# Kernel tuning notes

Hardware: AMD Instinct MI355X
Metric: run time of the kernel (lower is better)

Reference implementation:

```python
import jax, jax.numpy as jnp
import numpy as np

NUM_HEADS = 16
EPS = 1e-5


def _layernorm(x, gamma, beta):
    # LayerNorm over last dim (head_dim), biased variance as in torch
    mu = jnp.mean(x, axis=-1, keepdims=True)
    var = jnp.mean(jnp.square(x - mu), axis=-1, keepdims=True)
    return (x - mu) * jax.lax.rsqrt(var + EPS) * gamma + beta


def setup_inputs() -> dict:
    key = jax.random.key(0)
    ks = jax.random.split(key, 10)
    B, T, C = 16, 2048, 1024
    Bk = 4
    Dh = C // NUM_HEADS
    w = 0.02
    return {
        "q": jax.random.normal(ks[0], (B, T, C), jnp.float32),
        "k": jax.random.normal(ks[1], (Bk, T, C), jnp.float32),
        "v": jax.random.normal(ks[2], (Bk, T, C), jnp.float32),
        "Wq": jax.random.normal(ks[3], (C, C), jnp.float32) * w,
        "Wk": jax.random.normal(ks[4], (C, C), jnp.float32) * w,
        "Wv": jax.random.normal(ks[5], (C, C), jnp.float32) * w,
        "Wo": jax.random.normal(ks[6], (C, C), jnp.float32) * w,
        "bo": jnp.zeros((C,), jnp.float32),
        "gamma": jnp.ones((Dh,), jnp.float32),
        "beta": jnp.zeros((Dh,), jnp.float32),
    }


def reference(q, k, v, Wq, Wk, Wv, Wo, bo, gamma, beta):
    B, N, C = q.shape
    H = NUM_HEADS
    Dh = C // H
    scale = 8.0 / Dh  # use_mup=True

    reps = B // k.shape[0]
    k = jnp.tile(k, (reps, 1, 1))[:, :N]
    v = jnp.tile(v, (reps, 1, 1))[:, :N]

    # torch Linear: x @ W.T  (no qkv bias)
    qp = jnp.einsum("bnc,dc->bnd", q, Wq).reshape(B, N, H, Dh)
    kp = jnp.einsum("bnc,dc->bnd", k, Wk).reshape(B, N, H, Dh)
    vp = jnp.einsum("bnc,dc->bnd", v, Wv).reshape(B, N, H, Dh)

    qp = _layernorm(qp, gamma, beta) * scale
    kp = _layernorm(kp, gamma, beta)

    # Faithful to source: NO head permute before matmul -> per-token (H,H) attention
    attn = jnp.einsum("bnhd,bngd->bnhg", qp, kp)  # [B,N,H,H]
    attn = jax.nn.softmax(attn, axis=-1)
    x = jnp.einsum("bnhg,bngd->bnhd", attn, vp)  # [B,N,H,Dh]
    # torch: transpose(1,2).reshape(B,N,C)
    x = x.transpose(0, 2, 1, 3).reshape(B, N, C)
    return jnp.einsum("bnc,dc->bnd", x, Wo) + bo
```

## Files before the change

kernel.cpp:

```cpp
#include <hip/hip_runtime.h>
#include <stdint.h>

typedef short bf16x8 __attribute__((ext_vector_type(8)));
typedef float f32x4 __attribute__((ext_vector_type(4)));

#define DEVINL static __device__ __forceinline__
#define SB() __builtin_amdgcn_sched_barrier(0)

DEVINL unsigned short f2bf(float f) {
    union { float f; uint32_t u; } v; v.f = f;
    return (unsigned short)((v.u + 0x7FFFu + ((v.u >> 16) & 1u)) >> 16);
}
DEVINL float bf2f(unsigned short b) {
    union { uint32_t u; float f; } v; v.u = ((uint32_t)b) << 16;
    return v.f;
}

DEVINL void load_lds16(const void* g, void* l) {
    __builtin_amdgcn_global_load_lds(
        (const __attribute__((address_space(1))) void*)g,
        (__attribute__((address_space(3))) void*)l, 16, 0, 0);
}

__global__ __launch_bounds__(256) void k_cvt(const float* __restrict__ src,
                                             unsigned short* __restrict__ dst, int n4) {
    int stride = gridDim.x * blockDim.x;
    for (int i = blockIdx.x * blockDim.x + threadIdx.x; i < n4; i += stride) {
        float4 f = reinterpret_cast<const float4*>(src)[i];
        ushort4 o;
        o.x = f2bf(f.x); o.y = f2bf(f.y); o.z = f2bf(f.z); o.w = f2bf(f.w);
        reinterpret_cast<ushort4*>(dst)[i] = o;
    }
}

__global__ __launch_bounds__(256) void k_cvt2(
    const float* __restrict__ s0, const float* __restrict__ s1,
    unsigned short* __restrict__ d0, unsigned short* __restrict__ d1, int n4) {
    const int half = gridDim.x >> 1;
    const int sel = blockIdx.x < half ? 0 : 1;
    const float* src = sel ? s1 : s0;
    unsigned short* dst = sel ? d1 : d0;
    const int blk = blockIdx.x - sel * half;
    for (int i = blk * 256 + threadIdx.x; i < n4; i += half * 256) {
        float4 f = reinterpret_cast<const float4*>(src)[i];
        ushort4 o;
        o.x = f2bf(f.x); o.y = f2bf(f.y); o.z = f2bf(f.z); o.w = f2bf(f.w);
        reinterpret_cast<ushort4*>(dst)[i] = o;
    }
}

__global__ __launch_bounds__(256) void k_cvtW(
    const float* __restrict__ s0, const float* __restrict__ s1,
    const float* __restrict__ s2, const float* __restrict__ s3,
    unsigned short* __restrict__ d0, unsigned short* __restrict__ d1,
    unsigned short* __restrict__ d2, unsigned short* __restrict__ d3) {
    const float* srcs[4] = {s0, s1, s2, s3};
    unsigned short* dsts[4] = {d0, d1, d2, d3};
    const int wsel = blockIdx.x >> 8;
    const int blk  = blockIdx.x & 255;
    const float* src = srcs[wsel];
    unsigned short* dst = dsts[wsel];
    for (int i = blk * 256 + threadIdx.x; i < 262144; i += 65536) {
        float4 f = reinterpret_cast<const float4*>(src)[i];
        ushort4 o;
        o.x = f2bf(f.x); o.y = f2bf(f.y); o.z = f2bf(f.z); o.w = f2bf(f.w);
        reinterpret_cast<ushort4*>(dst)[i] = o;
    }
}

#define LOFF(buf, ab, ks, row) (((((buf) * 2 + (ab)) * 2 + (ks)) * 256 + (row)) * 32)

template<int EPI>
DEVINL void gemm256_body(
    const unsigned short* __restrict__ A,
    const unsigned short* __restrict__ B,
    void* __restrict__ Cout,
    const float* __restrict__ bias,
    const float* __restrict__ gamma,
    const float* __restrict__ beta,
    unsigned short* lds, int bid, int nwg, int tid)
{
    constexpr int K = 1024;
    constexpr int N = 1024;
    constexpr int NT = 16;

    const int wg  = (bid & 7) * (nwg >> 3) + (bid >> 3);
    const int m0 = (wg >> 2) * 256;
    const int n0 = (wg & 3) * 256;

    const int w = tid >> 6;
    const int lane = tid & 63;
    const int wr = w >> 2;
    const int wc = w & 3;

    const int srow = lane >> 2;
    const int sseg = lane & 3;
    const int sslot = sseg ^ ((srow >> 1) & 3);

    f32x4 acc[8][4] = {};

    auto stage_unit = [&](int buf, int kt, int unit) {
        const int k0 = kt * 64;
        const int ab = unit & 1;
        const int sel = unit >> 1;
        #pragma unroll
        for (int j = 0; j < 2; ++j) {
            const int c  = (w << 1) | j;
            const int ks = c >> 3;
            const int c3 = c & 7;
            const int rg = ab ? (sel * 2 + (c3 & 1) + ((c3 >> 1) << 2))
                              : (sel * 4 + (c3 & 3) + ((c3 >> 2) << 3));
            const int row = rg * 16 + srow;
            const unsigned short* src =
                (ab ? B + (size_t)(n0 + row) * K : A + (size_t)(m0 + row) * K)
                + k0 + ks * 32 + sslot * 8;
            load_lds16(src, lds + LOFF(buf, ab, ks, rg * 16));
        }
    };

    const int rr = lane & 15;
    const int rdslot = ((lane >> 4) ^ ((rr >> 1) & 3)) * 8;

    auto rd_a = [&](bf16x8 (&dst)[4][2], int cur, int mh) {
        #pragma unroll
        for (int i = 0; i < 4; ++i)
            #pragma unroll
            for (int ks = 0; ks < 2; ++ks)
                dst[i][ks] = *reinterpret_cast<const bf16x8*>(
                    lds + LOFF(cur, 0, ks, wr * 128 + mh * 64 + i * 16 + rr) + rdslot);
    };
    auto rd_b = [&](bf16x8 (&dst)[2][2], int cur, int nh) {
        #pragma unroll
        for (int j = 0; j < 2; ++j)
            #pragma unroll
            for (int ks = 0; ks < 2; ++ks)
                dst[j][ks] = *reinterpret_cast<const bf16x8*>(
                    lds + LOFF(cur, 1, ks, wc * 64 + nh * 32 + j * 16 + rr) + rdslot);
    };

    #define MFMA_QUAD(mi, nj, av, bv)                                          \
        __builtin_amdgcn_s_setprio(1);                                         \
        _Pragma("unroll")                                                      \
        for (int i = 0; i < 4; ++i)                                            \
            _Pragma("unroll")                                                  \
            for (int j = 0; j < 2; ++j)                                        \
                _Pragma("unroll")                                              \
                for (int ks = 0; ks < 2; ++ks)                                 \
                    acc[(mi) * 4 + i][(nj) * 2 + j] =                          \
                        __builtin_amdgcn_mfma_f32_16x16x32_bf16(               \
                            av[i][ks], bv[j][ks], acc[(mi)*4+i][(nj)*2+j], 0, 0, 0); \
        __builtin_amdgcn_s_setprio(0);

    stage_unit(0, 0, 0);
    stage_unit(0, 0, 1);
    stage_unit(0, 0, 3);
    stage_unit(0, 0, 2);
    asm volatile("s_waitcnt vmcnt(4)" ::: "memory");
    __builtin_amdgcn_s_barrier();
    SB();

    bf16x8 a[4][2], b0[2][2], b1[2][2];
    int cur = 0;
    for (int kt = 0; kt < NT - 1; ++kt) {
        const int nxt = cur ^ 1;

        rd_a(a, cur, 0);
        rd_b(b0, cur, 0);
        SB();
        stage_unit(nxt, kt + 1, 0);
        asm volatile("s_waitcnt vmcnt(4)" ::: "memory");
        __builtin_amdgcn_s_barrier();
        SB();
        asm volatile("s_waitcnt lgkmcnt(0)" ::: "memory");
        SB();
        MFMA_QUAD(0, 0, a, b0)

        rd_b(b1, cur, 1);
        SB();
        stage_unit(nxt, kt + 1, 1);
        asm volatile("s_waitcnt vmcnt(4)" ::: "memory");
        __builtin_amdgcn_s_barrier();
        SB();
        asm volatile("s_waitcnt lgkmcnt(0)" ::: "memory");
        SB();
        MFMA_QUAD(0, 1, a, b1)

        rd_a(a, cur, 1);
        SB();
        stage_unit(nxt, kt + 1, 3);
        __builtin_amdgcn_s_barrier();
        SB();
        asm volatile("s_waitcnt lgkmcnt(0)" ::: "memory");
        SB();
        MFMA_QUAD(1, 0, a, b0)

        stage_unit(nxt, kt + 1, 2);
        asm volatile("s_waitcnt vmcnt(4)" ::: "memory");
        __builtin_amdgcn_s_barrier();
        SB();
        MFMA_QUAD(1, 1, a, b1)
        cur = nxt;
    }

    {
        rd_a(a, cur, 0);
        rd_b(b0, cur, 0);
        SB();
        asm volatile("s_waitcnt vmcnt(2)" ::: "memory");
        __builtin_amdgcn_s_barrier();
        SB();
        asm volatile("s_waitcnt lgkmcnt(0)" ::: "memory");
        SB();
        MFMA_QUAD(0, 0, a, b0)

        rd_b(b1, cur, 1);
        SB();
        asm volatile("s_waitcnt vmcnt(0)" ::: "memory");
        __builtin_amdgcn_s_barrier();
        SB();
        asm volatile("s_waitcnt lgkmcnt(0)" ::: "memory");
        SB();
        MFMA_QUAD(0, 1, a, b1)

        rd_a(a, cur, 1);
        SB();
        asm volatile("s_waitcnt lgkmcnt(0)" ::: "memory");
        SB();
        MFMA_QUAD(1, 0, a, b0)
        MFMA_QUAD(1, 1, a, b1)
    }
    #undef MFMA_QUAD

    const int rg = lane >> 4;
    if constexpr (EPI == 0) {
        #pragma unroll
        for (int jj = 0; jj < 4; ++jj) {
            const int col = n0 + wc * 64 + jj * 16 + rr;
            const float bv = bias[col];
            #pragma unroll
            for (int i = 0; i < 8; ++i) {
                const int row0 = m0 + wr * 128 + i * 16 + rg * 4;
                #pragma unroll
                for (int r = 0; r < 4; ++r)
                    reinterpret_cast<float*>(Cout)[(size_t)(row0 + r) * N + col] =
                        acc[i][jj][r] + bv;
            }
        }
    } else if constexpr (EPI == 1 || EPI == 3) {
        const float scale = (EPI == 1) ? 0.125f : 1.0f;
        float gm[4], bt[4];
        #pragma unroll
        for (int jj = 0; jj < 4; ++jj) { gm[jj] = gamma[jj * 16 + rr]; bt[jj] = beta[jj * 16 + rr]; }
        #pragma unroll
        for (int i = 0; i < 8; ++i)
            #pragma unroll
            for (int r = 0; r < 4; ++r) {
                float s = 0.f, sq = 0.f;
                #pragma unroll
                for (int jj = 0; jj < 4; ++jj) {
                    const float v = acc[i][jj][r];
                    s += v; sq += v * v;
                }
                s  += __shfl_xor(s, 1);  s  += __shfl_xor(s, 2);
                s  += __shfl_xor(s, 4);  s  += __shfl_xor(s, 8);
                sq += __shfl_xor(sq, 1); sq += __shfl_xor(sq, 2);
                sq += __shfl_xor(sq, 4); sq += __shfl_xor(sq, 8);
                const float mu = s * 0.015625f;
                const float var = sq * 0.015625f - mu * mu;
                const float inv = rsqrtf(var + 1e-5f);
                const int row = m0 + wr * 128 + i * 16 + rg * 4 + r;
                #pragma unroll
                for (int jj = 0; jj < 4; ++jj) {
                    const int col = n0 + wc * 64 + jj * 16 + rr;
                    const float val = ((acc[i][jj][r] - mu) * inv * gm[jj] + bt[jj]) * scale;
                    reinterpret_cast<unsigned short*>(Cout)[(size_t)row * N + col] = f2bf(val);
                }
            }
    } else {
        const int g = (wg & 3) * 4 + wc;
        const int kqv = g >> 3;
        const int ev = g & 7;
        #pragma unroll
        for (int i = 0; i < 8; ++i)
            #pragma unroll
            for (int r = 0; r < 4; ++r) {
                const int t = m0 + wr * 128 + i * 16 + rg * 4 + r;
                #pragma unroll
                for (int jj = 0; jj < 4; ++jj)
                    reinterpret_cast<unsigned short*>(Cout)[
                        (size_t)t * 1024 + jj * 256 + kqv * 128 + rr * 8 + ev] =
                        f2bf(acc[i][jj][r]);
            }
    }
}

template<int EPI>
__global__ __launch_bounds__(512, 2) void k_gemm256(
    const unsigned short* __restrict__ A,
    const unsigned short* __restrict__ B,
    void* __restrict__ Cout,
    const float* __restrict__ bias,
    const float* __restrict__ gamma,
    const float* __restrict__ beta)
{
    __shared__ __align__(16) unsigned short lds[2 * 2 * 2 * 256 * 32];
    gemm256_body<EPI>(A, B, Cout, bias, gamma, beta, lds, blockIdx.x, gridDim.x, threadIdx.x);
}

__global__ __launch_bounds__(512, 2) void k_gemm256kv(
    const unsigned short* __restrict__ Ak,
    const unsigned short* __restrict__ Bk,
    void* __restrict__ Ck,
    const unsigned short* __restrict__ Av,
    const unsigned short* __restrict__ Bv,
    void* __restrict__ Cv,
    const float* __restrict__ gamma,
    const float* __restrict__ beta)
{
    __shared__ __align__(16) unsigned short lds[2 * 2 * 2 * 256 * 32];
    if (blockIdx.x < 128)
        gemm256_body<3>(Ak, Bk, Ck, nullptr, gamma, beta, lds, blockIdx.x, 128, threadIdx.x);
    else
        gemm256_body<2>(Av, Bv, Cv, nullptr, nullptr, nullptr, lds, blockIdx.x - 128, 128, threadIdx.x);
}

__global__ __launch_bounds__(256) void k_attn2(
    const unsigned short* __restrict__ qln,
    const unsigned short* __restrict__ kln,
    const unsigned short* __restrict__ vperm,
    unsigned short* __restrict__ xout)
{
    __shared__ unsigned short ps[4][256];
    __shared__ unsigned short xs[4][16 * 68];

    const int w = threadIdx.x >> 6;
    const int lane = threadIdx.x & 63;
    const int token = blockIdx.x * 4 + w;
    const int b = token >> 11;
    const int n = token & 2047;
    const int tokk = (b & 3) * 2048 + n;
    const int rr = lane & 15;
    const int kq = lane >> 4;

    const unsigned short* qp = qln + (size_t)token * 1024 + rr * 64 + kq * 8;
    const unsigned short* kp = kln + (size_t)tokk * 1024 + rr * 64 + kq * 8;
    const bf16x8 aq0 = *reinterpret_cast<const bf16x8*>(qp);
    const bf16x8 aq1 = *reinterpret_cast<const bf16x8*>(qp + 32);
    const bf16x8 bk0 = *reinterpret_cast<const bf16x8*>(kp);
    const bf16x8 bk1 = *reinterpret_cast<const bf16x8*>(kp + 32);
    f32x4 s = {};
    s = __builtin_amdgcn_mfma_f32_16x16x32_bf16(aq0, bk0, s, 0, 0, 0);
    s = __builtin_amdgcn_mfma_f32_16x16x32_bf16(aq1, bk1, s, 0, 0, 0);

    #pragma unroll
    for (int r = 0; r < 4; ++r) {
        float m = s[r];
        m = fmaxf(m, __shfl_xor(m, 1));
        m = fmaxf(m, __shfl_xor(m, 2));
        m = fmaxf(m, __shfl_xor(m, 4));
        m = fmaxf(m, __shfl_xor(m, 8));
        const float e = __expf(s[r] - m);
        float t = e;
        t += __shfl_xor(t, 1); t += __shfl_xor(t, 2);
        t += __shfl_xor(t, 4); t += __shfl_xor(t, 8);
        ps[w][(kq * 4 + r) * 16 + rr] = f2bf(e / t);
    }

    bf16x8 ap = {};
    if (kq < 2)
        ap = *reinterpret_cast<const bf16x8*>(&ps[w][rr * 16 + kq * 8]);

    const unsigned short* vp = vperm + (size_t)tokk * 1024;
    #pragma unroll
    for (int dblk = 0; dblk < 4; ++dblk) {
        bf16x8 bv = {};
        if (kq < 2)
            bv = *reinterpret_cast<const bf16x8*>(vp + dblk * 256 + kq * 128 + rr * 8);
        f32x4 z = {};
        const f32x4 x = __builtin_amdgcn_mfma_f32_16x16x32_bf16(ap, bv, z, 0, 0, 0);
        #pragma unroll
        for (int r = 0; r < 4; ++r)
            xs[w][(kq * 4 + r) * 68 + dblk * 16 + rr] = f2bf(x[r]);
    }

    const int h2 = lane >> 2;
    const int sg = lane & 3;
    const uint4 lo = *reinterpret_cast<const uint4*>(&xs[w][h2 * 68 + sg * 16]);
    const uint4 hi = *reinterpret_cast<const uint4*>(&xs[w][h2 * 68 + sg * 16 + 8]);
    unsigned short* dst = xout + (size_t)b * 2048 * 1024 +
                          (size_t)(h2 * 128 + (n >> 4)) * 1024 + (n & 15) * 64 + sg * 16;
    *reinterpret_cast<uint4*>(dst) = lo;
    *reinterpret_cast<uint4*>(dst + 8) = hi;
}

extern "C" void kernel_launch(void* const* d_in, const int* in_sizes, int n_in,
                              void* d_out, int out_size, void* d_ws, size_t ws_size,
                              hipStream_t stream) {
    const float* q     = (const float*)d_in[0];
    const float* k     = (const float*)d_in[1];
    const float* v     = (const float*)d_in[2];
    const float* Wq    = (const float*)d_in[3];
    const float* Wk    = (const float*)d_in[4];
    const float* Wv    = (const float*)d_in[5];
    const float* Wo    = (const float*)d_in[6];
    const float* bo    = (const float*)d_in[7];
    const float* gamma = (const float*)d_in[8];
    const float* beta  = (const float*)d_in[9];
    float* out = (float*)d_out;

    char* ws = (char*)d_ws;
    const size_t MB = 1024 * 1024;
    unsigned short* qb    = (unsigned short*)(ws + 0);
    unsigned short* xsc   = (unsigned short*)(ws + 0);
    unsigned short* qpb   = (unsigned short*)(ws + 64 * MB);
    unsigned short* klnb  = (unsigned short*)(ws + 128 * MB);
    unsigned short* vbb   = (unsigned short*)(ws + 144 * MB);
    unsigned short* vpm   = (unsigned short*)(ws + 160 * MB);
    unsigned short* kbb   = (unsigned short*)(ws + 176 * MB);
    unsigned short* Wkb   = (unsigned short*)(ws + 192 * MB);
    unsigned short* Wvb   = (unsigned short*)(ws + 194 * MB);
    unsigned short* Wqb   = (unsigned short*)(ws + 196 * MB);
    unsigned short* Wob   = (unsigned short*)(ws + 198 * MB);

    k_cvtW<<<1024, 256, 0, stream>>>(Wk, Wv, Wq, Wo, Wkb, Wvb, Wqb, Wob);

    k_cvt2<<<2048, 256, 0, stream>>>(k, v, kbb, vbb, 2097152);

    k_gemm256kv<<<256, 512, 0, stream>>>(kbb, Wkb, klnb, vbb, Wvb, vpm, gamma, beta);

    k_cvt<<<2048, 256, 0, stream>>>(q, qb, 8388608);

    k_gemm256<1><<<512, 512, 0, stream>>>(qb, Wqb, qpb, nullptr, gamma, beta);

    k_attn2<<<8192, 256, 0, stream>>>(qpb, klnb, vpm, xsc);

    k_gemm256<0><<<512, 512, 0, stream>>>(xsc, Wob, out, bo, nullptr, nullptr);
}
```

Measured before the change: 307.9 us.

## Merge all fp32→bf16 conversions into one launch; single-buffer Q/O GEMMs for occupancy

Folds the q, k, v and four weight conversions into a single kernel launch, which removes launch overhead and tail gaps between the small conversion kernels. Adds a single-buffered LDS variant of the 256x256 GEMM with launch bounds of 4 blocks per CU, used for the Q projection and output projection. The idea is to halve LDS per block so more blocks can be resident and latency is hidden across blocks rather than by double buffering within one. The cost is that loads for the next k-tile no longer overlap the current tile's MFMAs inside a block, and the tighter launch bound may cause register spills with the 8x4 accumulator tile.

```diff
diff --git a/kernel.cpp b/kernel.cpp
--- a/kernel.cpp
+++ b/kernel.cpp
@@ -22,10 +22,27 @@
         (__attribute__((address_space(3))) void*)l, 16, 0, 0);
 }
 
-__global__ __launch_bounds__(256) void k_cvt(const float* __restrict__ src,
-                                             unsigned short* __restrict__ dst, int n4) {
-    int stride = gridDim.x * blockDim.x;
-    for (int i = blockIdx.x * blockDim.x + threadIdx.x; i < n4; i += stride) {
+__global__ __launch_bounds__(256) void k_cvtall(
+    const float* __restrict__ q, const float* __restrict__ k, const float* __restrict__ v,
+    const float* __restrict__ w0, const float* __restrict__ w1,
+    const float* __restrict__ w2, const float* __restrict__ w3,
+    unsigned short* __restrict__ dq, unsigned short* __restrict__ dk,
+    unsigned short* __restrict__ dv,
+    unsigned short* __restrict__ dw0, unsigned short* __restrict__ dw1,
+    unsigned short* __restrict__ dw2, unsigned short* __restrict__ dw3)
+{
+    const float* src; unsigned short* dst; int n4, blk, nblk;
+    const int b = blockIdx.x;
+    if (b < 2048)      { src = q; dst = dq; n4 = 8388608; blk = b;        nblk = 2048; }
+    else if (b < 2560) { src = k; dst = dk; n4 = 2097152; blk = b - 2048; nblk = 512; }
+    else if (b < 3072) { src = v; dst = dv; n4 = 2097152; blk = b - 2560; nblk = 512; }
+    else {
+        const int wsel = (b - 3072) >> 6;
+        const float* ws_[4] = {w0, w1, w2, w3};
+        unsigned short* wd_[4] = {dw0, dw1, dw2, dw3};
+        src = ws_[wsel]; dst = wd_[wsel]; n4 = 262144; blk = (b - 3072) & 63; nblk = 64;
+    }
+    for (int i = blk * 256 + threadIdx.x; i < n4; i += nblk * 256) {
         float4 f = reinterpret_cast<const float4*>(src)[i];
         ushort4 o;
         o.x = f2bf(f.x); o.y = f2bf(f.y); o.z = f2bf(f.z); o.w = f2bf(f.w);
@@ -33,204 +50,26 @@
     }
 }
 
-__global__ __launch_bounds__(256) void k_cvt2(
-    const float* __restrict__ s0, const float* __restrict__ s1,
-    unsigned short* __restrict__ d0, unsigned short* __restrict__ d1, int n4) {
-    const int half = gridDim.x >> 1;
-    const int sel = blockIdx.x < half ? 0 : 1;
-    const float* src = sel ? s1 : s0;
-    unsigned short* dst = sel ? d1 : d0;
-    const int blk = blockIdx.x - sel * half;
-    for (int i = blk * 256 + threadIdx.x; i < n4; i += half * 256) {
-        float4 f = reinterpret_cast<const float4*>(src)[i];
-        ushort4 o;
-        o.x = f2bf(f.x); o.y = f2bf(f.y); o.z = f2bf(f.z); o.w = f2bf(f.w);
-        reinterpret_cast<ushort4*>(dst)[i] = o;
-    }
-}
-
-__global__ __launch_bounds__(256) void k_cvtW(
-    const float* __restrict__ s0, const float* __restrict__ s1,
-    const float* __restrict__ s2, const float* __restrict__ s3,
-    unsigned short* __restrict__ d0, unsigned short* __restrict__ d1,
-    unsigned short* __restrict__ d2, unsigned short* __restrict__ d3) {
-    const float* srcs[4] = {s0, s1, s2, s3};
-    unsigned short* dsts[4] = {d0, d1, d2, d3};
-    const int wsel = blockIdx.x >> 8;
-    const int blk  = blockIdx.x & 255;
-    const float* src = srcs[wsel];
-    unsigned short* dst = dsts[wsel];
-    for (int i = blk * 256 + threadIdx.x; i < 262144; i += 65536) {
-        float4 f = reinterpret_cast<const float4*>(src)[i];
-        ushort4 o;
-        o.x = f2bf(f.x); o.y = f2bf(f.y); o.z = f2bf(f.z); o.w = f2bf(f.w);
-        reinterpret_cast<ushort4*>(dst)[i] = o;
-    }
-}
-
-#define LOFF(buf, ab, ks, row) (((((buf) * 2 + (ab)) * 2 + (ks)) * 256 + (row)) * 32)
+#define MFMA_QUAD(mi, nj, av, bv)                                              \
+    __builtin_amdgcn_s_setprio(1);                                             \
+    _Pragma("unroll")                                                          \
+    for (int i = 0; i < 4; ++i)                                                \
+        _Pragma("unroll")                                                      \
+        for (int j = 0; j < 2; ++j)                                            \
+            _Pragma("unroll")                                                  \
+            for (int ks = 0; ks < 2; ++ks)                                     \
+                acc[(mi) * 4 + i][(nj) * 2 + j] =                              \
+                    __builtin_amdgcn_mfma_f32_16x16x32_bf16(                   \
+                        av[i][ks], bv[j][ks], acc[(mi)*4+i][(nj)*2+j], 0, 0, 0); \
+    __builtin_amdgcn_s_setprio(0);
 
 template<int EPI>
-DEVINL void gemm256_body(
-    const unsigned short* __restrict__ A,
-    const unsigned short* __restrict__ B,
-    void* __restrict__ Cout,
-    const float* __restrict__ bias,
-    const float* __restrict__ gamma,
-    const float* __restrict__ beta,
-    unsigned short* lds, int bid, int nwg, int tid)
-{
-    constexpr int K = 1024;
+DEVINL void epi_write(f32x4 (&acc)[8][4], void* Cout,
+                      const float* bias, const float* gamma, const float* beta,
+                      int m0, int n0, int wr, int wc, int lane, int wg)
+{
     constexpr int N = 1024;
-    constexpr int NT = 16;
-
-    const int wg  = (bid & 7) * (nwg >> 3) + (bid >> 3);
-    const int m0 = (wg >> 2) * 256;
-    const int n0 = (wg & 3) * 256;
-
-    const int w = tid >> 6;
-    const int lane = tid & 63;
-    const int wr = w >> 2;
-    const int wc = w & 3;
-
-    const int srow = lane >> 2;
-    const int sseg = lane & 3;
-    const int sslot = sseg ^ ((srow >> 1) & 3);
-
-    f32x4 acc[8][4] = {};
-
-    auto stage_unit = [&](int buf, int kt, int unit) {
-        const int k0 = kt * 64;
-        const int ab = unit & 1;
-        const int sel = unit >> 1;
-        #pragma unroll
-        for (int j = 0; j < 2; ++j) {
-            const int c  = (w << 1) | j;
-            const int ks = c >> 3;
-            const int c3 = c & 7;
-            const int rg = ab ? (sel * 2 + (c3 & 1) + ((c3 >> 1) << 2))
-                              : (sel * 4 + (c3 & 3) + ((c3 >> 2) << 3));
-            const int row = rg * 16 + srow;
-            const unsigned short* src =
-                (ab ? B + (size_t)(n0 + row) * K : A + (size_t)(m0 + row) * K)
-                + k0 + ks * 32 + sslot * 8;
-            load_lds16(src, lds + LOFF(buf, ab, ks, rg * 16));
-        }
-    };
-
     const int rr = lane & 15;
-    const int rdslot = ((lane >> 4) ^ ((rr >> 1) & 3)) * 8;
-
-    auto rd_a = [&](bf16x8 (&dst)[4][2], int cur, int mh) {
-        #pragma unroll
-        for (int i = 0; i < 4; ++i)
-            #pragma unroll
-            for (int ks = 0; ks < 2; ++ks)
-                dst[i][ks] = *reinterpret_cast<const bf16x8*>(
-                    lds + LOFF(cur, 0, ks, wr * 128 + mh * 64 + i * 16 + rr) + rdslot);
-    };
-    auto rd_b = [&](bf16x8 (&dst)[2][2], int cur, int nh) {
-        #pragma unroll
-        for (int j = 0; j < 2; ++j)
-            #pragma unroll
-            for (int ks = 0; ks < 2; ++ks)
-                dst[j][ks] = *reinterpret_cast<const bf16x8*>(
-                    lds + LOFF(cur, 1, ks, wc * 64 + nh * 32 + j * 16 + rr) + rdslot);
-    };
-
-    #define MFMA_QUAD(mi, nj, av, bv)                                          \
-        __builtin_amdgcn_s_setprio(1);                                         \
-        _Pragma("unroll")                                                      \
-        for (int i = 0; i < 4; ++i)                                            \
-            _Pragma("unroll")                                                  \
-            for (int j = 0; j < 2; ++j)                                        \
-                _Pragma("unroll")                                              \
-                for (int ks = 0; ks < 2; ++ks)                                 \
-                    acc[(mi) * 4 + i][(nj) * 2 + j] =                          \
-                        __builtin_amdgcn_mfma_f32_16x16x32_bf16(               \
-                            av[i][ks], bv[j][ks], acc[(mi)*4+i][(nj)*2+j], 0, 0, 0); \
-        __builtin_amdgcn_s_setprio(0);
-
-    stage_unit(0, 0, 0);
-    stage_unit(0, 0, 1);
-    stage_unit(0, 0, 3);
-    stage_unit(0, 0, 2);
-    asm volatile("s_waitcnt vmcnt(4)" ::: "memory");
-    __builtin_amdgcn_s_barrier();
-    SB();
-
-    bf16x8 a[4][2], b0[2][2], b1[2][2];
-    int cur = 0;
-    for (int kt = 0; kt < NT - 1; ++kt) {
-        const int nxt = cur ^ 1;
-
-        rd_a(a, cur, 0);
-        rd_b(b0, cur, 0);
-        SB();
-        stage_unit(nxt, kt + 1, 0);
-        asm volatile("s_waitcnt vmcnt(4)" ::: "memory");
-        __builtin_amdgcn_s_barrier();
-        SB();
-        asm volatile("s_waitcnt lgkmcnt(0)" ::: "memory");
-        SB();
-        MFMA_QUAD(0, 0, a, b0)
-
-        rd_b(b1, cur, 1);
-        SB();
-        stage_unit(nxt, kt + 1, 1);
-        asm volatile("s_waitcnt vmcnt(4)" ::: "memory");
-        __builtin_amdgcn_s_barrier();
-        SB();
-        asm volatile("s_waitcnt lgkmcnt(0)" ::: "memory");
-        SB();
-        MFMA_QUAD(0, 1, a, b1)
-
-        rd_a(a, cur, 1);
-        SB();
-        stage_unit(nxt, kt + 1, 3);
-        __builtin_amdgcn_s_barrier();
-        SB();
-        asm volatile("s_waitcnt lgkmcnt(0)" ::: "memory");
-        SB();
-        MFMA_QUAD(1, 0, a, b0)
-
-        stage_unit(nxt, kt + 1, 2);
-        asm volatile("s_waitcnt vmcnt(4)" ::: "memory");
-        __builtin_amdgcn_s_barrier();
-        SB();
-        MFMA_QUAD(1, 1, a, b1)
-        cur = nxt;
-    }
-
-    {
-        rd_a(a, cur, 0);
-        rd_b(b0, cur, 0);
-        SB();
-        asm volatile("s_waitcnt vmcnt(2)" ::: "memory");
-        __builtin_amdgcn_s_barrier();
-        SB();
-        asm volatile("s_waitcnt lgkmcnt(0)" ::: "memory");
-        SB();
-        MFMA_QUAD(0, 0, a, b0)
-
-        rd_b(b1, cur, 1);
-        SB();
-        asm volatile("s_waitcnt vmcnt(0)" ::: "memory");
-        __builtin_amdgcn_s_barrier();
-        SB();
-        asm volatile("s_waitcnt lgkmcnt(0)" ::: "memory");
-        SB();
-        MFMA_QUAD(0, 1, a, b1)
-
-        rd_a(a, cur, 1);
-        SB();
-        asm volatile("s_waitcnt lgkmcnt(0)" ::: "memory");
-        SB();
-        MFMA_QUAD(1, 0, a, b0)
-        MFMA_QUAD(1, 1, a, b1)
-    }
-    #undef MFMA_QUAD
-
     const int rg = lane >> 4;
     if constexpr (EPI == 0) {
         #pragma unroll
@@ -294,8 +133,267 @@
     }
 }
 
+#define LOFF(buf, ab, ks, row) (((((buf) * 2 + (ab)) * 2 + (ks)) * 256 + (row)) * 32)
+
 template<int EPI>
-__global__ __launch_bounds__(512, 2) void k_gemm256(
+DEVINL void gemm256_body(
+    const unsigned short* __restrict__ A,
+    const unsigned short* __restrict__ B,
+    void* __restrict__ Cout,
+    const float* __restrict__ bias,
+    const float* __restrict__ gamma,
+    const float* __restrict__ beta,
+    unsigned short* lds, int bid, int nwg, int tid)
+{
+    constexpr int K = 1024;
+    constexpr int NT = 16;
+
+    const int wg  = (bid & 7) * (nwg >> 3) + (bid >> 3);
+    const int m0 = (wg >> 2) * 256;
+    const int n0 = (wg & 3) * 256;
+
+    const int w = tid >> 6;
+    const int lane = tid & 63;
+    const int wr = w >> 2;
+    const int wc = w & 3;
+
+    const int srow = lane >> 2;
+    const int sseg = lane & 3;
+    const int sslot = sseg ^ ((srow >> 1) & 3);
+
+    f32x4 acc[8][4] = {};
+
+    auto stage_unit = [&](int buf, int kt, int unit) {
+        const int k0 = kt * 64;
+        const int ab = unit & 1;
+        const int sel = unit >> 1;
+        #pragma unroll
+        for (int j = 0; j < 2; ++j) {
+            const int c  = (w << 1) | j;
+            const int ks = c >> 3;
+            const int c3 = c & 7;
+            const int rg = ab ? (sel * 2 + (c3 & 1) + ((c3 >> 1) << 2))
+                              : (sel * 4 + (c3 & 3) + ((c3 >> 2) << 3));
+            const int row = rg * 16 + srow;
+            const unsigned short* src =
+                (ab ? B + (size_t)(n0 + row) * K : A + (size_t)(m0 + row) * K)
+                + k0 + ks * 32 + sslot * 8;
+            load_lds16(src, lds + LOFF(buf, ab, ks, rg * 16));
+        }
+    };
+
+    const int rr = lane & 15;
+    const int rdslot = ((lane >> 4) ^ ((rr >> 1) & 3)) * 8;
+
+    auto rd_a = [&](bf16x8 (&dst)[4][2], int cur, int mh) {
+        #pragma unroll
+        for (int i = 0; i < 4; ++i)
+            #pragma unroll
+            for (int ks = 0; ks < 2; ++ks)
+                dst[i][ks] = *reinterpret_cast<const bf16x8*>(
+                    lds + LOFF(cur, 0, ks, wr * 128 + mh * 64 + i * 16 + rr) + rdslot);
+    };
+    auto rd_b = [&](bf16x8 (&dst)[2][2], int cur, int nh) {
+        #pragma unroll
+        for (int j = 0; j < 2; ++j)
+            #pragma unroll
+            for (int ks = 0; ks < 2; ++ks)
+                dst[j][ks] = *reinterpret_cast<const bf16x8*>(
+                    lds + LOFF(cur, 1, ks, wc * 64 + nh * 32 + j * 16 + rr) + rdslot);
+    };
+
+    stage_unit(0, 0, 0);
+    stage_unit(0, 0, 1);
+    stage_unit(0, 0, 3);
+    stage_unit(0, 0, 2);
+    asm volatile("s_waitcnt vmcnt(4)" ::: "memory");
+    __builtin_amdgcn_s_barrier();
+    SB();
+
+    bf16x8 a[4][2], b0[2][2], b1[2][2];
+    int cur = 0;
+    for (int kt = 0; kt < NT - 1; ++kt) {
+        const int nxt = cur ^ 1;
+
+        rd_a(a, cur, 0);
+        rd_b(b0, cur, 0);
+        SB();
+        stage_unit(nxt, kt + 1, 0);
+        asm volatile("s_waitcnt vmcnt(4)" ::: "memory");
+        __builtin_amdgcn_s_barrier();
+        SB();
+        asm volatile("s_waitcnt lgkmcnt(0)" ::: "memory");
+        SB();
+        MFMA_QUAD(0, 0, a, b0)
+
+        rd_b(b1, cur, 1);
+        SB();
+        stage_unit(nxt, kt + 1, 1);
+        asm volatile("s_waitcnt vmcnt(4)" ::: "memory");
+        __builtin_amdgcn_s_barrier();
+        SB();
+        asm volatile("s_waitcnt lgkmcnt(0)" ::: "memory");
+        SB();
+        MFMA_QUAD(0, 1, a, b1)
+
+        rd_a(a, cur, 1);
+        SB();
+        stage_unit(nxt, kt + 1, 3);
+        __builtin_amdgcn_s_barrier();
+        SB();
+        asm volatile("s_waitcnt lgkmcnt(0)" ::: "memory");
+        SB();
+        MFMA_QUAD(1, 0, a, b0)
+
+        stage_unit(nxt, kt + 1, 2);
+        asm volatile("s_waitcnt vmcnt(4)" ::: "memory");
+        __builtin_amdgcn_s_barrier();
+        SB();
+        MFMA_QUAD(1, 1, a, b1)
+        cur = nxt;
+    }
+
+    {
+        rd_a(a, cur, 0);
+        rd_b(b0, cur, 0);
+        SB();
+        asm volatile("s_waitcnt vmcnt(2)" ::: "memory");
+        __builtin_amdgcn_s_barrier();
+        SB();
+        asm volatile("s_waitcnt lgkmcnt(0)" ::: "memory");
+        SB();
+        MFMA_QUAD(0, 0, a, b0)
+
+        rd_b(b1, cur, 1);
+        SB();
+        asm volatile("s_waitcnt vmcnt(0)" ::: "memory");
+        __builtin_amdgcn_s_barrier();
+        SB();
+        asm volatile("s_waitcnt lgkmcnt(0)" ::: "memory");
+        SB();
+        MFMA_QUAD(0, 1, a, b1)
+
+        rd_a(a, cur, 1);
+        SB();
+        asm volatile("s_waitcnt lgkmcnt(0)" ::: "memory");
+        SB();
+        MFMA_QUAD(1, 0, a, b0)
+        MFMA_QUAD(1, 1, a, b1)
+    }
+
+    epi_write<EPI>(acc, Cout, bias, gamma, beta, m0, n0, wr, wc, lane, wg);
+}
+
+#define LOFFS(ab, ks, row) ((((ab) * 2 + (ks)) * 256 + (row)) * 32)
+
+template<int EPI>
+DEVINL void gemm256s_body(
+    const unsigned short* __restrict__ A,
+    const unsigned short* __restrict__ B,
+    void* __restrict__ Cout,
+    const float* __restrict__ bias,
+    const float* __restrict__ gamma,
+    const float* __restrict__ beta,
+    unsigned short* lds, int bid, int nwg, int tid)
+{
+    constexpr int K = 1024;
+    constexpr int NT = 16;
+
+    const int wg  = (bid & 7) * (nwg >> 3) + (bid >> 3);
+    const int m0 = (wg >> 2) * 256;
+    const int n0 = (wg & 3) * 256;
+
+    const int w = tid >> 6;
+    const int lane = tid & 63;
+    const int wr = w >> 2;
+    const int wc = w & 3;
+
+    const int srow = lane >> 2;
+    const int sseg = lane & 3;
+    const int sslot = sseg ^ ((srow >> 1) & 3);
+
+    f32x4 acc[8][4] = {};
+
+    auto stage_all = [&](int kt) {
+        const int k0 = kt * 64;
+        #pragma unroll
+        for (int unit = 0; unit < 4; ++unit) {
+            const int ab = unit & 1;
+            const int sel = unit >> 1;
+            #pragma unroll
+            for (int j = 0; j < 2; ++j) {
+                const int c  = (w << 1) | j;
+                const int ks = c >> 3;
+                const int c3 = c & 7;
+                const int rg = ab ? (sel * 2 + (c3 & 1) + ((c3 >> 1) << 2))
+                                  : (sel * 4 + (c3 & 3) + ((c3 >> 2) << 3));
+                const int row = rg * 16 + srow;
+                const unsigned short* src =
+                    (ab ? B + (size_t)(n0 + row) * K : A + (size_t)(m0 + row) * K)
+                    + k0 + ks * 32 + sslot * 8;
+                load_lds16(src, lds + LOFFS(ab, ks, rg * 16));
+            }
+        }
+    };
+
+    const int rr = lane & 15;
+    const int rdslot = ((lane >> 4) ^ ((rr >> 1) & 3)) * 8;
+
+    auto rd_a = [&](bf16x8 (&dst)[4][2], int mh) {
+        #pragma unroll
+        for (int i = 0; i < 4; ++i)
+            #pragma unroll
+            for (int ks = 0; ks < 2; ++ks)
+                dst[i][ks] = *reinterpret_cast<const bf16x8*>(
+                    lds + LOFFS(0, ks, wr * 128 + mh * 64 + i * 16 + rr) + rdslot);
+    };
+    auto rd_b = [&](bf16x8 (&dst)[2][2], int nh) {
+        #pragma unroll
+        for (int j = 0; j < 2; ++j)
+            #pragma unroll
+            for (int ks = 0; ks < 2; ++ks)
+                dst[j][ks] = *reinterpret_cast<const bf16x8*>(
+                    lds + LOFFS(1, ks, wc * 64 + nh * 32 + j * 16 + rr) + rdslot);
+    };
+
+    stage_all(0);
+
+    bf16x8 a[4][2], b0[2][2], b1[2][2];
+    for (int kt = 0; kt < NT; ++kt) {
+        asm volatile("s_waitcnt vmcnt(0)" ::: "memory");
+        SB();
+        __builtin_amdgcn_s_barrier();
+        SB();
+        rd_a(a, 0);
+        rd_b(b0, 0);
+        rd_b(b1, 1);
+        SB();
+        asm volatile("s_waitcnt lgkmcnt(4)" ::: "memory");
+        SB();
+        MFMA_QUAD(0, 0, a, b0)
+        asm volatile("s_waitcnt lgkmcnt(0)" ::: "memory");
+        SB();
+        MFMA_QUAD(0, 1, a, b1)
+        rd_a(a, 1);
+        SB();
+        asm volatile("s_waitcnt lgkmcnt(0)" ::: "memory");
+        SB();
+        MFMA_QUAD(1, 0, a, b0)
+        MFMA_QUAD(1, 1, a, b1)
+        if (kt + 1 < NT) {
+            __builtin_amdgcn_s_barrier();
+            SB();
+            stage_all(kt + 1);
+        }
+    }
+
+    epi_write<EPI>(acc, Cout, bias, gamma, beta, m0, n0, wr, wc, lane, wg);
+}
+
+#undef MFMA_QUAD
+
+template<int EPI>
+__global__ __launch_bounds__(512, 4) void k_gemm256s(
     const unsigned short* __restrict__ A,
     const unsigned short* __restrict__ B,
     void* __restrict__ Cout,
@@ -303,8 +401,8 @@
     const float* __restrict__ gamma,
     const float* __restrict__ beta)
 {
-    __shared__ __align__(16) unsigned short lds[2 * 2 * 2 * 256 * 32];
-    gemm256_body<EPI>(A, B, Cout, bias, gamma, beta, lds, blockIdx.x, gridDim.x, threadIdx.x);
+    __shared__ __align__(16) unsigned short lds[2 * 2 * 256 * 32];
+    gemm256s_body<EPI>(A, B, Cout, bias, gamma, beta, lds, blockIdx.x, gridDim.x, threadIdx.x);
 }
 
 __global__ __launch_bounds__(512, 2) void k_gemm256kv(
@@ -422,17 +520,14 @@
     unsigned short* Wqb   = (unsigned short*)(ws + 196 * MB);
     unsigned short* Wob   = (unsigned short*)(ws + 198 * MB);
 
-    k_cvtW<<<1024, 256, 0, stream>>>(Wk, Wv, Wq, Wo, Wkb, Wvb, Wqb, Wob);
-
-    k_cvt2<<<2048, 256, 0, stream>>>(k, v, kbb, vbb, 2097152);
+    k_cvtall<<<3328, 256, 0, stream>>>(q, k, v, Wk, Wv, Wq, Wo,
+                                       qb, kbb, vbb, Wkb, Wvb, Wqb, Wob);
 
     k_gemm256kv<<<256, 512, 0, stream>>>(kbb, Wkb, klnb, vbb, Wvb, vpm, gamma, beta);
 
-    k_cvt<<<2048, 256, 0, stream>>>(q, qb, 8388608);
-
-    k_gemm256<1><<<512, 512, 0, stream>>>(qb, Wqb, qpb, nullptr, gamma, beta);
+    k_gemm256s<1><<<512, 512, 0, stream>>>(qb, Wqb, qpb, nullptr, gamma, beta);
 
     k_attn2<<<8192, 256, 0, stream>>>(qpb, klnb, vpm, xsc);
 
-    k_gemm256<0><<<512, 512, 0, stream>>>(xsc, Wob, out, bo, nullptr, nullptr);
-}
+    k_gemm256s<0><<<512, 512, 0, stream>>>(xsc, Wob, out, bo, nullptr, nullptr);
+}
```

After: 1.178 ms. 3.83x slower.
